# Kernel optimization log

Hardware: AMD Instinct MI355X
Metric: run time of the kernel (lower is better)

The kernel has to match this reference:

```python
import jax, jax.numpy as jnp
import numpy as np

B, H, W = 512, 15, 15
DF, DP, DV, DD = 64, 32, 64, 32
PM = 16
NUM_LINE = 442503  # get_total_num_line_encoding(11)


def fake_quant(x, scale=128., num_bits=8, floor=False):
    qmin = float(-(2 ** (num_bits - 1)))
    qmax = float(2 ** (num_bits - 1) - 1)
    xs = jnp.clip(x * scale, qmin, qmax)
    q = jnp.floor(xs) if floor else jnp.round(xs)
    q = xs + jax.lax.stop_gradient(q - xs)  # straight-through estimator
    return q / scale


def qw(w):  # LinearBlock quant=True weight: int8 at scale 128
    return fake_quant(w, 128., 8)


def qb(b):  # LinearBlock quant=True bias: int32 at scale 128*128
    return fake_quant(b, 128. * 128., 32)


def setup_inputs() -> dict:
    key = jax.random.key(0)
    ks = jax.random.split(key, 24)
    n = lambda k, shape, s=0.1: jax.random.normal(k, shape, dtype=jnp.float32) * s
    return {
        'line_encoding': jax.random.randint(ks[0], (B, 4, H, W), 0, NUM_LINE, dtype=jnp.int32),
        'emb': n(ks[1], (NUM_LINE, DF), 0.5),
        'dw_w': n(ks[2], (DD, 3, 3)),
        'dw_b': n(ks[3], (DD,)),
        'pw1_w': n(ks[4], (DP * 2, DF)), 'pw1_b': n(ks[5], (DP * 2,)),
        'pw2_w': n(ks[6], (PM * DP + PM, DP * 2)), 'pw2_b': n(ks[7], (PM * DP + PM,)),
        'pout_w': n(ks[8], (PM,), 0.2), 'pout_b': n(ks[9], (1,), 0.2),
        'star_up1_w': n(ks[10], (4, DV, DF)), 'star_up1_b': n(ks[11], (4, DV)),
        'star_up2_w': n(ks[12], (4, DV, DF)), 'star_up2_b': n(ks[13], (4, DV)),
        'star_down_w': n(ks[14], (4, DV, DV)), 'star_down_b': n(ks[15], (4, DV)),
        'vl1_w': n(ks[16], (DV, DF + 4 * DV)), 'vl1_b': n(ks[17], (DV,)),
        'vl2_w': n(ks[18], (DV, DV)), 'vl2_b': n(ks[19], (DV,)),
        'vl3_w': n(ks[20], (3, DV)), 'vl3_b': n(ks[21], (3,)),
    }


def _star(x, w1, b1, w2, b2, w3, b3):
    # x: [B,R,DF]; weights [R,DV,DF] (per-region parameter gather)
    x1 = jnp.einsum('brc,rdc->brd', x, qw(w1)) + qb(b1)[None]
    x2 = jnp.einsum('brc,rdc->brd', x, qw(w2)) + qb(b2)[None]
    h = jax.nn.relu(x1) * x2  # star operation
    return jnp.einsum('brc,rdc->brd', h, qw(w3)) + qb(b3)[None]


def _forward(line_encoding, emb, dw_w, dw_b, pw1_w, pw1_b, pw2_w, pw2_b,
             pout_w, pout_b, star_up1_w, star_up1_b, star_up2_w, star_up2_b,
             star_down_w, star_down_b, vl1_w, vl1_b, vl2_w, vl2_b, vl3_w, vl3_b):
    # ---- feature: embedding gather + quant + direction mean ----
    f = emb[line_encoding]                       # [B,4,H,W,DF]
    f = jnp.clip(f, -16., 16.)
    f = fake_quant(f, 32., 16)
    f = jax.nn.relu(jnp.mean(f, axis=1))         # [B,H,W,DF]
    f = jnp.transpose(f, (0, 3, 1, 2))           # [B,DF,H,W]
    # ---- depthwise 3x3 conv, quant='pixel-dwconv-floor' ----
    x = fake_quant(f[:, :DD] * 4., 128., 16)
    wq = fake_quant(dw_w, 65536., 16)
    bq = fake_quant(dw_b, 128., 16)
    xp = jnp.pad(x, ((0, 0), (0, 0), (1, 1), (1, 1)))
    pat = jnp.stack([xp[:, :, dy:dy + H, dx:dx + W]
                     for dy in range(3) for dx in range(3)], axis=2)  # [B,DD,9,H,W]
    prod = fake_quant(pat * wq.reshape(1, DD, 9, 1, 1), 128., 32, floor=True)
    conv = jax.nn.relu(prod.sum(axis=2) + bq.reshape(1, DD, 1, 1))
    feat_dw = fake_quant(conv, 128., 16)
    feat_dir = fake_quant(f[:, DD:], 128., 16)
    feature = jnp.concatenate([feat_dw, feat_dir], axis=1)  # [B,DF,H,W]
    # ---- global and 3x3 regional sums ----
    feature_sum = fake_quant(feature.sum(axis=(2, 3)) / 256., 128., 32, floor=True)
    Hs = [0, H // 3 + (H % 3 == 2), H // 3 * 2 + (H % 3 > 0), H]
    Ws = [0, W // 3 + (W % 3 == 2), W // 3 * 2 + (W % 3 > 0), W]
    regions = jnp.stack([feature[:, :, Hs[i]:Hs[i + 1], Ws[j]:Ws[j + 1]].sum(axis=(2, 3))
                         for i in range(3) for j in range(3)], axis=1)  # [B,9,DF]
    regions = fake_quant(regions / 32., 128., 32, floor=True)
    # ---- policy: dynamic per-sample pointwise conv ----
    h = jax.nn.relu(feature_sum @ qw(pw1_w).T + qb(pw1_b))
    o = h @ qw(pw2_w).T + qb(pw2_b)                         # [B, PM*DP+PM]
    pw = fake_quant(o[:, :PM * DP], 128. * 128., 16, floor=True).reshape(-1, PM, DP)
    pin = fake_quant(feature[:, :DP], 128., 16)             # [B,DP,H,W]
    pol = jnp.einsum('bchw,bic->bihw', pin, pw)             # grouped conv, groups=B
    pbias = o[:, PM * DP:].reshape(-1, PM, 1, 1)
    pol = jax.nn.relu(pol + pbias)
    policy = jnp.einsum('bihw,i->bhw', pol, pout_w)[:, None] + pout_b[0]  # [B,1,H,W]
    # ---- value: corner/edge/center star blocks over 9 regions ----
    idx = jnp.array([0, 1, 0, 1, 2, 1, 0, 1, 0])  # 0=corner,1=edge,2=center
    v = _star(regions, star_up1_w[idx], star_up1_b[idx], star_up2_w[idx],
              star_up2_b[idx], star_down_w[idx], star_down_b[idx])  # [B,9,DV]
    fq8 = lambda t: fake_quant(t, 128., 8, floor=True)
    def avg4(a, b, c, d):
        a, b, c, d = fq8(a), fq8(b), fq8(c), fq8(d)
        ab = fq8((a + b + 1. / 128.) / 2.)
        cd = fq8((c + d + 1. / 128.) / 2.)
        return fq8((ab + cd + 1. / 128.) / 2.)
    quads = jnp.stack([avg4(v[:, 0], v[:, 1], v[:, 3], v[:, 4]),
                       avg4(v[:, 1], v[:, 2], v[:, 4], v[:, 5]),
                       avg4(v[:, 3], v[:, 4], v[:, 6], v[:, 7]),
                       avg4(v[:, 4], v[:, 5], v[:, 7], v[:, 8])], axis=1)  # [B,4,DV]
    qidx = jnp.array([3, 3, 3, 3])  # value_quad shared across quadrants
    vq = _star(quads, star_up1_w[qidx], star_up1_b[qidx], star_up2_w[qidx],
               star_up2_b[qidx], star_down_w[qidx], star_down_b[qidx])  # [B,4,DV]
    value = jnp.concatenate([feature_sum, vq.reshape(vq.shape[0], -1)], axis=1)  # [B,320]
    value = jax.nn.relu(value @ qw(vl1_w).T + qb(vl1_b))
    value = jax.nn.relu(value @ qw(vl2_w).T + qb(vl2_b))
    value = value @ qw(vl3_w).T + qb(vl3_b)                 # [B,3]
    return value, policy


def reference(line_encoding, emb, dw_w, dw_b, pw1_w, pw1_b, pw2_w, pw2_b,
              pout_w, pout_b, star_up1_w, star_up1_b, star_up2_w, star_up2_b,
              star_down_w, star_down_b, vl1_w, vl1_b, vl2_w, vl2_b, vl3_w, vl3_b):
    return _forward(line_encoding, emb, dw_w, dw_b, pw1_w, pw1_b, pw2_w, pw2_b,
                    pout_w, pout_b, star_up1_w, star_up1_b, star_up2_w, star_up2_b,
                    star_down_w, star_down_b, vl1_w, vl1_b, vl2_w, vl2_b, vl3_w, vl3_b)
```

## Files before the change

kernel.cpp:

```cpp
#include <hip/hip_runtime.h>

#define NPOS 225
#define FSTR 226

#define OFF_PW1Q 0
#define OFF_PW2Q 4096
#define OFF_SU1Q 37888
#define OFF_SU2Q 54272
#define OFF_SDQ  70656
#define OFF_VL1Q 87040
#define OFF_VL2Q 107520
#define OFF_VL3Q 111616
#define OFF_PW1B 111808
#define OFF_PW2B 111872
#define OFF_SU1B 112400
#define OFF_SU2B 112656
#define OFF_SDB  112912
#define OFF_VL1B 113168
#define OFF_VL2B 113232
#define OFF_VL3B 113296
#define OFF_DWW  113300
#define OFF_DWB  113588
#define WS_TOTAL 113620

__device__ __forceinline__ float qw8(float w) {
  return rintf(fminf(fmaxf(w * 128.f, -128.f), 127.f)) * 0.0078125f;
}
__device__ __forceinline__ float qb32(float b) {
  return rintf(b * 16384.f) * 6.103515625e-05f;
}
__device__ __forceinline__ float fq8f(float v) {
  return floorf(fminf(fmaxf(v * 128.f, -128.f), 127.f)) * 0.0078125f;
}
__device__ __forceinline__ float qd32(float v) {
  return rintf(fminf(fmaxf(v, -16.f), 16.f) * 32.f);
}

__global__ void nnue_prep(const float* __restrict__ pw1_w, const float* __restrict__ pw1_b,
                          const float* __restrict__ pw2_w, const float* __restrict__ pw2_b,
                          const float* __restrict__ su1w,  const float* __restrict__ su1b,
                          const float* __restrict__ su2w,  const float* __restrict__ su2b,
                          const float* __restrict__ sdw,   const float* __restrict__ sdb,
                          const float* __restrict__ vl1w,  const float* __restrict__ vl1b,
                          const float* __restrict__ vl2w,  const float* __restrict__ vl2b,
                          const float* __restrict__ vl3w,  const float* __restrict__ vl3b,
                          const float* __restrict__ dw_w,  const float* __restrict__ dw_b,
                          float* __restrict__ wsf, int* __restrict__ wsi)
{
  const int i = blockIdx.x * 256 + threadIdx.x;
  if (i < 111808) {
    const float* src; int off;
    if      (i < 4096)   { src = pw1_w; off = 0; }
    else if (i < 37888)  { src = pw2_w; off = 4096; }
    else if (i < 54272)  { src = su1w;  off = 37888; }
    else if (i < 70656)  { src = su2w;  off = 54272; }
    else if (i < 87040)  { src = sdw;   off = 70656; }
    else if (i < 107520) { src = vl1w;  off = 87040; }
    else if (i < 111616) { src = vl2w;  off = 107520; }
    else                 { src = vl3w;  off = 111616; }
    wsf[i] = qw8(src[i - off]);
  } else if (i < 113299) {
    const int j = i - 111808;
    const float* src; int off;
    if      (j < 64)   { src = pw1_b; off = 0; }
    else if (j < 592)  { src = pw2_b; off = 64; }
    else if (j < 848)  { src = su1b;  off = 592; }
    else if (j < 1104) { src = su2b;  off = 848; }
    else if (j < 1360) { src = sdb;   off = 1104; }
    else if (j < 1424) { src = vl1b;  off = 1360; }
    else if (j < 1488) { src = vl2b;  off = 1424; }
    else               { src = vl3b;  off = 1488; }
    wsf[i] = qb32(src[j - off]);
  } else if (i >= 113300 && i < 113588) {
    wsi[i] = (int)rintf(fminf(fmaxf(dw_w[i - 113300] * 65536.f, -32768.f), 32767.f));
  } else if (i >= 113588 && i < 113620) {
    wsi[i] = (int)rintf(fminf(fmaxf(dw_b[i - 113588] * 128.f, -32768.f), 32767.f));
  }
}

__global__ __launch_bounds__(256, 3)
void nnue_main(const int* __restrict__ line, const float* __restrict__ emb,
               const float* __restrict__ pout_w, const float* __restrict__ pout_b,
               const float* __restrict__ wsf, const int* __restrict__ wsi,
               float* __restrict__ out)
{
  __shared__ unsigned short fbuf[64 * FSTR];
  __shared__ int sle[900];
  __shared__ float sreg[576];
  __shared__ float sfsum[64];
  __shared__ float shh[64];
  __shared__ float sobuf[528];
  __shared__ float spwq[512];
  __shared__ float hstar[576];
  __shared__ float vstar[576];
  __shared__ float squads[256];
  __shared__ float shq[256];
  __shared__ float svq[256];
  __shared__ float sv1[64];
  __shared__ float sv2[64];

  const int tid  = threadIdx.x;
  const int b    = blockIdx.x;
  const int wid  = tid >> 6;
  const int lane = tid & 63;
  const int* le  = line + b * 4 * NPOS;

  for (int i = tid; i < 900; i += 256) sle[i] = le[i];
  __syncthreads();

  const int start = (wid * NPOS) >> 2;
  const int end   = ((wid + 1) * NPOS) >> 2;
  for (int p0 = start; p0 < end; p0 += 8) {
    float vv[32];
#pragma unroll
    for (int j = 0; j < 8; ++j) {
      int pp = p0 + j; if (pp >= end) pp = end - 1;
#pragma unroll
      for (int d = 0; d < 4; ++d) {
        const int idx = __builtin_amdgcn_readfirstlane(sle[d * NPOS + pp]);
        vv[j * 4 + d] = emb[(size_t)(unsigned)idx * 64u + (unsigned)lane];
      }
    }
#pragma unroll
    for (int j = 0; j < 8; ++j) {
      const int pp = p0 + j;
      if (pp < end) {
        float s = qd32(vv[4 * j]) + qd32(vv[4 * j + 1]) + qd32(vv[4 * j + 2]) + qd32(vv[4 * j + 3]);
        fbuf[lane * FSTR + pp] = (unsigned short)fmaxf(s, 0.f);
      }
    }
  }
  __syncthreads();

  {
    const int cc = tid >> 3;
    const int pg = tid & 7;
    int w9[9];
#pragma unroll
    for (int t = 0; t < 9; ++t) w9[t] = wsi[OFF_DWW + cc * 9 + t];
    const int bqi = wsi[OFF_DWB + cc];
    const unsigned short* frow = &fbuf[cc * FSTR];
    int outr[29];
#pragma unroll
    for (int k = 0; k < 29; ++k) {
      const int p = pg + 8 * k;
      int res = 0;
      if (p < NPOS) {
        const int y0 = (p * 2185) >> 15;
        const int x0 = p - y0 * 15;
        const int ym = (y0 > 0), yp = (y0 < 14), xm = (x0 > 0), xp = (x0 < 14);
        int acc = 0;
#pragma unroll
        for (int dy = 0; dy < 3; ++dy) {
          const int vy = (dy == 0) ? ym : ((dy == 2) ? yp : 1);
#pragma unroll
          for (int dx = 0; dx < 3; ++dx) {
            const int vx = (dx == 0) ? xm : ((dx == 2) ? xp : 1);
            int q = p + (dy - 1) * 15 + (dx - 1);
            q = (q < 0) ? 0 : ((q > 224) ? 224 : q);
            int kk = frow[q];
            kk = (vy && vx) ? kk : 0;
            acc += (kk * 4 * w9[dy * 3 + dx]) >> 16;
          }
        }
        res = acc + bqi;
        res = res < 0 ? 0 : res;
        res = res > 32767 ? 32767 : res;
      }
      outr[k] = res;
    }
    __syncthreads();
#pragma unroll
    for (int k = 0; k < 29; ++k) {
      const int p = pg + 8 * k;
      if (p < NPOS) fbuf[cc * FSTR + p] = (unsigned short)outr[k];
    }
  }
  __syncthreads();

  {
    int* sregKi = (int*)sreg;
    for (int task = tid; task < 576; task += 256) {
      const int r = task >> 6, c = task & 63;
      const int rh = (r * 11) >> 5;
      const int rw = r - rh * 3;
      const unsigned short* fr = &fbuf[c * FSTR + rh * 75 + rw * 5];
      int K = 0;
#pragma unroll
      for (int y = 0; y < 5; ++y)
#pragma unroll
        for (int x = 0; x < 5; ++x) K += fr[y * 15 + x];
      sregKi[task] = K;
    }
  }
  __syncthreads();
  if (tid < 64) {
    int* sregKi = (int*)sreg;
    int Ks[9], tot = 0;
#pragma unroll
    for (int r = 0; r < 9; ++r) { Ks[r] = sregKi[r * 64 + tid]; tot += Ks[r]; }
#pragma unroll
    for (int r = 0; r < 9; ++r) sreg[r * 64 + tid] = (float)(Ks[r] >> 5) * 0.0078125f;
    sfsum[tid] = (float)(tot >> 8) * 0.0078125f;
  }
  __syncthreads();

  if (tid < 64) {
    const float4* wr = (const float4*)(wsf + OFF_PW1Q + tid * 64);
    float acc = 0.f;
#pragma unroll
    for (int c4 = 0; c4 < 16; ++c4) {
      float4 w = wr[c4];
      acc += sfsum[c4 * 4 + 0] * w.x;
      acc += sfsum[c4 * 4 + 1] * w.y;
      acc += sfsum[c4 * 4 + 2] * w.z;
      acc += sfsum[c4 * 4 + 3] * w.w;
    }
    shh[tid] = fmaxf(acc + wsf[OFF_PW1B + tid], 0.f);
  }
  __syncthreads();
  for (int j = tid; j < 528; j += 256) {
    const float4* wr = (const float4*)(wsf + OFF_PW2Q + j * 64);
    float acc = 0.f;
#pragma unroll
    for (int c4 = 0; c4 < 16; ++c4) {
      float4 w = wr[c4];
      acc += shh[c4 * 4 + 0] * w.x;
      acc += shh[c4 * 4 + 1] * w.y;
      acc += shh[c4 * 4 + 2] * w.z;
      acc += shh[c4 * 4 + 3] * w.w;
    }
    acc += wsf[OFF_PW2B + j];
    sobuf[j] = acc;
    if (j < 512)
      spwq[j] = floorf(fminf(fmaxf(acc * 16384.f, -32768.f), 32767.f)) * 6.103515625e-05f;
  }
  __syncthreads();

  if (tid < NPOS) {
    float pinv[32];
#pragma unroll
    for (int c = 0; c < 32; ++c) pinv[c] = (float)fbuf[c * FSTR + tid] * 0.0078125f;
    float acc = 0.f;
#pragma unroll
    for (int i = 0; i < 16; ++i) {
      float s = 0.f;
#pragma unroll
      for (int c = 0; c < 32; ++c) s += pinv[c] * spwq[i * 32 + c];
      s = fmaxf(s + sobuf[512 + i], 0.f);
      acc += s * pout_w[i];
    }
    out[1536 + b * NPOS + tid] = acc + pout_b[0];
  }

  {
    const int g = tid >> 6;
    const int d = tid & 63;
    int ty, rA, rB, rC, rD;
    if (g == 0)      { ty = 0; rA = 0; rB = 2; rC = 6; rD = 8; }
    else if (g == 1) { ty = 1; rA = 1; rB = 3; rC = 5; rD = 7; }
    else             { ty = 2; rA = 4; rB = 4; rC = 4; rD = 4; }
    const float4* w1r = (const float4*)(wsf + OFF_SU1Q + ty * 4096 + d * 64);
    const float4* w2r = (const float4*)(wsf + OFF_SU2Q + ty * 4096 + d * 64);
    float aA1 = 0, aB1 = 0, aC1 = 0, aD1 = 0, aA2 = 0, aB2 = 0, aC2 = 0, aD2 = 0;
#pragma unroll 4
    for (int c4 = 0; c4 < 16; ++c4) {
      float4 w1 = w1r[c4], w2 = w2r[c4];
      float q1[4] = {w1.x, w1.y, w1.z, w1.w};
      float q2[4] = {w2.x, w2.y, w2.z, w2.w};
#pragma unroll
      for (int u = 0; u < 4; ++u) {
        const int c = c4 * 4 + u;
        float xA = sreg[rA * 64 + c], xB = sreg[rB * 64 + c];
        float xC = sreg[rC * 64 + c], xD = sreg[rD * 64 + c];
        aA1 += xA * q1[u]; aB1 += xB * q1[u]; aC1 += xC * q1[u]; aD1 += xD * q1[u];
        aA2 += xA * q2[u]; aB2 += xB * q2[u]; aC2 += xC * q2[u]; aD2 += xD * q2[u];
      }
    }
    const float bb1 = wsf[OFF_SU1B + ty * 64 + d];
    const float bb2 = wsf[OFF_SU2B + ty * 64 + d];
    hstar[rA * 64 + d] = fmaxf(aA1 + bb1, 0.f) * (aA2 + bb2);
    hstar[rB * 64 + d] = fmaxf(aB1 + bb1, 0.f) * (aB2 + bb2);
    hstar[rC * 64 + d] = fmaxf(aC1 + bb1, 0.f) * (aC2 + bb2);
    hstar[rD * 64 + d] = fmaxf(aD1 + bb1, 0.f) * (aD2 + bb2);
    __syncthreads();
    const float4* wdr = (const float4*)(wsf + OFF_SDQ + ty * 4096 + d * 64);
    float dA = 0, dB = 0, dC = 0, dD = 0;
#pragma unroll 4
    for (int c4 = 0; c4 < 16; ++c4) {
      float4 w = wdr[c4];
      float q[4] = {w.x, w.y, w.z, w.w};
#pragma unroll
      for (int u = 0; u < 4; ++u) {
        const int c = c4 * 4 + u;
        dA += hstar[rA * 64 + c] * q[u]; dB += hstar[rB * 64 + c] * q[u];
        dC += hstar[rC * 64 + c] * q[u]; dD += hstar[rD * 64 + c] * q[u];
      }
    }
    const float bd = wsf[OFF_SDB + ty * 64 + d];
    vstar[rA * 64 + d] = dA + bd;
    vstar[rB * 64 + d] = dB + bd;
    vstar[rC * 64 + d] = dC + bd;
    vstar[rD * 64 + d] = dD + bd;
  }
  __syncthreads();

  {
    const int g = tid >> 6, d = tid & 63;
    int r0, r1, r2v, r3v;
    if (g == 0)      { r0 = 0; r1 = 1; r2v = 3; r3v = 4; }
    else if (g == 1) { r0 = 1; r1 = 2; r2v = 4; r3v = 5; }
    else if (g == 2) { r0 = 3; r1 = 4; r2v = 6; r3v = 7; }
    else             { r0 = 4; r1 = 5; r2v = 7; r3v = 8; }
    float a  = fq8f(vstar[r0 * 64 + d]);
    float bb = fq8f(vstar[r1 * 64 + d]);
    float cc = fq8f(vstar[r2v * 64 + d]);
    float dd = fq8f(vstar[r3v * 64 + d]);
    float ab = fq8f((a + bb + 0.0078125f) * 0.5f);
    float cd = fq8f((cc + dd + 0.0078125f) * 0.5f);
    squads[g * 64 + d] = fq8f((ab + cd + 0.0078125f) * 0.5f);
  }
  __syncthreads();

  {
    const int g = tid >> 6, d = tid & 63;
    const float4* w1r = (const float4*)(wsf + OFF_SU1Q + 3 * 4096 + d * 64);
    const float4* w2r = (const float4*)(wsf + OFF_SU2Q + 3 * 4096 + d * 64);
    float a1 = 0.f, a2 = 0.f;
#pragma unroll 4
    for (int c4 = 0; c4 < 16; ++c4) {
      float4 w1 = w1r[c4], w2 = w2r[c4];
      float xq0 = squads[g * 64 + c4 * 4 + 0], xq1 = squads[g * 64 + c4 * 4 + 1];
      float xq2 = squads[g * 64 + c4 * 4 + 2], xq3 = squads[g * 64 + c4 * 4 + 3];
      a1 += xq0 * w1.x + xq1 * w1.y + xq2 * w1.z + xq3 * w1.w;
      a2 += xq0 * w2.x + xq1 * w2.y + xq2 * w2.z + xq3 * w2.w;
    }
    shq[g * 64 + d] = fmaxf(a1 + wsf[OFF_SU1B + 192 + d], 0.f) * (a2 + wsf[OFF_SU2B + 192 + d]);
    __syncthreads();
    const float4* wdr = (const float4*)(wsf + OFF_SDQ + 3 * 4096 + d * 64);
    float ad = 0.f;
#pragma unroll 4
    for (int c4 = 0; c4 < 16; ++c4) {
      float4 w = wdr[c4];
      ad += shq[g * 64 + c4 * 4 + 0] * w.x + shq[g * 64 + c4 * 4 + 1] * w.y
          + shq[g * 64 + c4 * 4 + 2] * w.z + shq[g * 64 + c4 * 4 + 3] * w.w;
    }
    svq[g * 64 + d] = ad + wsf[OFF_SDB + 192 + d];
  }
  __syncthreads();

  if (tid < 64) {
    const float4* wr = (const float4*)(wsf + OFF_VL1Q + tid * 320);
    float acc = 0.f;
#pragma unroll 4
    for (int k4 = 0; k4 < 16; ++k4) {
      float4 w = wr[k4];
      acc += sfsum[k4 * 4 + 0] * w.x;
      acc += sfsum[k4 * 4 + 1] * w.y;
      acc += sfsum[k4 * 4 + 2] * w.z;
      acc += sfsum[k4 * 4 + 3] * w.w;
    }
#pragma unroll 4
    for (int k4 = 16; k4 < 80; ++k4) {
      float4 w = wr[k4];
      const int base = k4 * 4 - 64;
      acc += svq[base + 0] * w.x;
      acc += svq[base + 1] * w.y;
      acc += svq[base + 2] * w.z;
      acc += svq[base + 3] * w.w;
    }
    sv1[tid] = fmaxf(acc + wsf[OFF_VL1B + tid], 0.f);
  }
  __syncthreads();
  if (tid < 64) {
    const float4* wr = (const float4*)(wsf + OFF_VL2Q + tid * 64);
    float acc = 0.f;
#pragma unroll 4
    for (int k4 = 0; k4 < 16; ++k4) {
      float4 w = wr[k4];
      acc += sv1[k4 * 4 + 0] * w.x;
      acc += sv1[k4 * 4 + 1] * w.y;
      acc += sv1[k4 * 4 + 2] * w.z;
      acc += sv1[k4 * 4 + 3] * w.w;
    }
    sv2[tid] = fmaxf(acc + wsf[OFF_VL2B + tid], 0.f);
  }
  __syncthreads();
  if (tid < 3) {
    const float* wr = wsf + OFF_VL3Q + tid * 64;
    float acc = 0.f;
#pragma unroll
    for (int k = 0; k < 64; ++k) acc += sv2[k] * wr[k];
    out[b * 3 + tid] = acc + wsf[OFF_VL3B + tid];
  }
}

extern "C" void kernel_launch(void* const* d_in, const int* in_sizes, int n_in,
                              void* d_out, int out_size, void* d_ws, size_t ws_size,
                              hipStream_t stream) {
  (void)in_sizes; (void)n_in; (void)out_size; (void)ws_size;
  float* wsf = (float*)d_ws;
  int*   wsi = (int*)d_ws;
  nnue_prep<<<(WS_TOTAL + 255) / 256, 256, 0, stream>>>(
      (const float*)d_in[4],  (const float*)d_in[5],
      (const float*)d_in[6],  (const float*)d_in[7],
      (const float*)d_in[10], (const float*)d_in[11],
      (const float*)d_in[12], (const float*)d_in[13],
      (const float*)d_in[14], (const float*)d_in[15],
      (const float*)d_in[16], (const float*)d_in[17],
      (const float*)d_in[18], (const float*)d_in[19],
      (const float*)d_in[20], (const float*)d_in[21],
      (const float*)d_in[2],  (const float*)d_in[3],
      wsf, wsi);
  nnue_main<<<512, 256, 0, stream>>>(
      (const int*)d_in[0], (const float*)d_in[1],
      (const float*)d_in[8], (const float*)d_in[9],
      wsf, wsi, (float*)d_out);
}
```

Baseline: 260.1 us.

## Double block to 512 threads and run policy and value branches concurrently

Raises the workgroup to 512 threads (8 waves). Embedding gather now uses 8 waves, reads line indices directly from global memory instead of staging them in LDS, and issues all 32 index loads before the embedding loads. The upper 4 waves compute the star value branch while the lower waves run the policy pw1/pw2/output layers, so the two branches overlap instead of running serially. This adds register pressure under the new launch bounds and some extra barriers, and leaves many threads idle in the tail layers.

```diff
diff --git a/kernel.cpp b/kernel.cpp
--- a/kernel.cpp
+++ b/kernel.cpp
@@ -78,14 +78,13 @@
   }
 }
 
-__global__ __launch_bounds__(256, 3)
+__global__ __launch_bounds__(512, 4)
 void nnue_main(const int* __restrict__ line, const float* __restrict__ emb,
                const float* __restrict__ pout_w, const float* __restrict__ pout_b,
                const float* __restrict__ wsf, const int* __restrict__ wsi,
                float* __restrict__ out)
 {
   __shared__ unsigned short fbuf[64 * FSTR];
-  __shared__ int sle[900];
   __shared__ float sreg[576];
   __shared__ float sfsum[64];
   __shared__ float shh[64];
@@ -101,49 +100,47 @@
 
   const int tid  = threadIdx.x;
   const int b    = blockIdx.x;
-  const int wid  = tid >> 6;
+  const int wid  = __builtin_amdgcn_readfirstlane(tid >> 6);
   const int lane = tid & 63;
   const int* le  = line + b * 4 * NPOS;
 
-  for (int i = tid; i < 900; i += 256) sle[i] = le[i];
-  __syncthreads();
-
-  const int start = (wid * NPOS) >> 2;
-  const int end   = ((wid + 1) * NPOS) >> 2;
-  for (int p0 = start; p0 < end; p0 += 8) {
-    float vv[32];
-#pragma unroll
-    for (int j = 0; j < 8; ++j) {
-      int pp = p0 + j; if (pp >= end) pp = end - 1;
-#pragma unroll
-      for (int d = 0; d < 4; ++d) {
-        const int idx = __builtin_amdgcn_readfirstlane(sle[d * NPOS + pp]);
-        vv[j * 4 + d] = emb[(size_t)(unsigned)idx * 64u + (unsigned)lane];
-      }
-    }
-#pragma unroll
-    for (int j = 0; j < 8; ++j) {
-      const int pp = p0 + j;
-      if (pp < end) {
-        float s = qd32(vv[4 * j]) + qd32(vv[4 * j + 1]) + qd32(vv[4 * j + 2]) + qd32(vv[4 * j + 3]);
-        fbuf[lane * FSTR + pp] = (unsigned short)fmaxf(s, 0.f);
-      }
-    }
-  }
-  __syncthreads();
-
   {
-    const int cc = tid >> 3;
-    const int pg = tid & 7;
+    const int s = (wid * NPOS) >> 3;
+    const int e = ((wid + 1) * NPOS) >> 3;
+    for (int p0 = s; p0 < e; p0 += 8) {
+      int idx[32];
+#pragma unroll
+      for (int j = 0; j < 8; ++j) {
+        int pp = p0 + j; pp = (pp < e) ? pp : (e - 1);
+#pragma unroll
+        for (int d = 0; d < 4; ++d) idx[j * 4 + d] = le[d * NPOS + pp];
+      }
+      float vv[32];
+#pragma unroll
+      for (int t = 0; t < 32; ++t)
+        vv[t] = emb[(unsigned)(idx[t] * 64 + lane)];
+#pragma unroll
+      for (int j = 0; j < 8; ++j) {
+        int pp = p0 + j; pp = (pp < e) ? pp : (e - 1);
+        float sm = qd32(vv[4 * j]) + qd32(vv[4 * j + 1]) + qd32(vv[4 * j + 2]) + qd32(vv[4 * j + 3]);
+        fbuf[lane * FSTR + pp] = (unsigned short)fmaxf(sm, 0.f);
+      }
+    }
+  }
+  __syncthreads();
+
+  {
+    const int cc = tid >> 4;
+    const int pg = tid & 15;
     int w9[9];
 #pragma unroll
     for (int t = 0; t < 9; ++t) w9[t] = wsi[OFF_DWW + cc * 9 + t];
     const int bqi = wsi[OFF_DWB + cc];
     const unsigned short* frow = &fbuf[cc * FSTR];
-    int outr[29];
-#pragma unroll
-    for (int k = 0; k < 29; ++k) {
-      const int p = pg + 8 * k;
+    int outr[15];
+#pragma unroll
+    for (int k = 0; k < 15; ++k) {
+      const int p = pg + 16 * k;
       int res = 0;
       if (p < NPOS) {
         const int y0 = (p * 2185) >> 15;
@@ -171,8 +168,8 @@
     }
     __syncthreads();
 #pragma unroll
-    for (int k = 0; k < 29; ++k) {
-      const int p = pg + 8 * k;
+    for (int k = 0; k < 15; ++k) {
+      const int p = pg + 16 * k;
       if (p < NPOS) fbuf[cc * FSTR + p] = (unsigned short)outr[k];
     }
   }
@@ -180,7 +177,7 @@
 
   {
     int* sregKi = (int*)sreg;
-    for (int task = tid; task < 576; task += 256) {
+    for (int task = tid; task < 576; task += 512) {
       const int r = task >> 6, c = task & 63;
       const int rh = (r * 11) >> 5;
       const int rw = r - rh * 3;
@@ -211,102 +208,108 @@
 #pragma unroll
     for (int c4 = 0; c4 < 16; ++c4) {
       float4 w = wr[c4];
-      acc += sfsum[c4 * 4 + 0] * w.x;
-      acc += sfsum[c4 * 4 + 1] * w.y;
-      acc += sfsum[c4 * 4 + 2] * w.z;
-      acc += sfsum[c4 * 4 + 3] * w.w;
+      acc += sfsum[c4 * 4 + 0] * w.x + sfsum[c4 * 4 + 1] * w.y
+           + sfsum[c4 * 4 + 2] * w.z + sfsum[c4 * 4 + 3] * w.w;
     }
     shh[tid] = fmaxf(acc + wsf[OFF_PW1B + tid], 0.f);
-  }
-  __syncthreads();
-  for (int j = tid; j < 528; j += 256) {
-    const float4* wr = (const float4*)(wsf + OFF_PW2Q + j * 64);
-    float acc = 0.f;
-#pragma unroll
-    for (int c4 = 0; c4 < 16; ++c4) {
-      float4 w = wr[c4];
-      acc += shh[c4 * 4 + 0] * w.x;
-      acc += shh[c4 * 4 + 1] * w.y;
-      acc += shh[c4 * 4 + 2] * w.z;
-      acc += shh[c4 * 4 + 3] * w.w;
-    }
-    acc += wsf[OFF_PW2B + j];
-    sobuf[j] = acc;
-    if (j < 512)
-      spwq[j] = floorf(fminf(fmaxf(acc * 16384.f, -32768.f), 32767.f)) * 6.103515625e-05f;
-  }
-  __syncthreads();
-
-  if (tid < NPOS) {
-    float pinv[32];
-#pragma unroll
-    for (int c = 0; c < 32; ++c) pinv[c] = (float)fbuf[c * FSTR + tid] * 0.0078125f;
-    float acc = 0.f;
-#pragma unroll
-    for (int i = 0; i < 16; ++i) {
-      float s = 0.f;
-#pragma unroll
-      for (int c = 0; c < 32; ++c) s += pinv[c] * spwq[i * 32 + c];
-      s = fmaxf(s + sobuf[512 + i], 0.f);
-      acc += s * pout_w[i];
-    }
-    out[1536 + b * NPOS + tid] = acc + pout_b[0];
-  }
-
-  {
-    const int g = tid >> 6;
+  } else if (tid >= 256) {
+    const int g = (tid >> 6) - 4;
+    const int d = tid & 63;
+    int ty, rA, rB, rC, rD;
+    if (g == 0)      { ty = 0; rA = 0; rB = 2; rC = 6; rD = 8; }
+    else if (g == 1) { ty = 1; rA = 1; rB = 3; rC = 5; rD = 7; }
+    else if (g == 2) { ty = 2; rA = 4; rB = 4; rC = 4; rD = 4; }
+    else             { ty = 3; rA = 4; rB = 4; rC = 4; rD = 4; }
+    if (g < 3) {
+      const float4* w1r = (const float4*)(wsf + OFF_SU1Q + ty * 4096 + d * 64);
+      const float4* w2r = (const float4*)(wsf + OFF_SU2Q + ty * 4096 + d * 64);
+      float aA1 = 0, aB1 = 0, aC1 = 0, aD1 = 0, aA2 = 0, aB2 = 0, aC2 = 0, aD2 = 0;
+#pragma unroll 4
+      for (int c4 = 0; c4 < 16; ++c4) {
+        float4 w1 = w1r[c4], w2 = w2r[c4];
+        float q1[4] = {w1.x, w1.y, w1.z, w1.w};
+        float q2[4] = {w2.x, w2.y, w2.z, w2.w};
+#pragma unroll
+        for (int u = 0; u < 4; ++u) {
+          const int c = c4 * 4 + u;
+          float xA = sreg[rA * 64 + c], xB = sreg[rB * 64 + c];
+          float xC = sreg[rC * 64 + c], xD = sreg[rD * 64 + c];
+          aA1 += xA * q1[u]; aB1 += xB * q1[u]; aC1 += xC * q1[u]; aD1 += xD * q1[u];
+          aA2 += xA * q2[u]; aB2 += xB * q2[u]; aC2 += xC * q2[u]; aD2 += xD * q2[u];
+        }
+      }
+      const float bb1 = wsf[OFF_SU1B + ty * 64 + d];
+      const float bb2 = wsf[OFF_SU2B + ty * 64 + d];
+      hstar[rA * 64 + d] = fmaxf(aA1 + bb1, 0.f) * (aA2 + bb2);
+      hstar[rB * 64 + d] = fmaxf(aB1 + bb1, 0.f) * (aB2 + bb2);
+      hstar[rC * 64 + d] = fmaxf(aC1 + bb1, 0.f) * (aC2 + bb2);
+      hstar[rD * 64 + d] = fmaxf(aD1 + bb1, 0.f) * (aD2 + bb2);
+    }
+  }
+  __syncthreads();
+
+  if (tid < 256) {
+    for (int j = tid; j < 528; j += 256) {
+      const float4* wr = (const float4*)(wsf + OFF_PW2Q + j * 64);
+      float acc = 0.f;
+#pragma unroll
+      for (int c4 = 0; c4 < 16; ++c4) {
+        float4 w = wr[c4];
+        acc += shh[c4 * 4 + 0] * w.x + shh[c4 * 4 + 1] * w.y
+             + shh[c4 * 4 + 2] * w.z + shh[c4 * 4 + 3] * w.w;
+      }
+      acc += wsf[OFF_PW2B + j];
+      sobuf[j] = acc;
+      if (j < 512)
+        spwq[j] = floorf(fminf(fmaxf(acc * 16384.f, -32768.f), 32767.f)) * 6.103515625e-05f;
+    }
+  } else {
+    const int g = (tid >> 6) - 4;
     const int d = tid & 63;
     int ty, rA, rB, rC, rD;
     if (g == 0)      { ty = 0; rA = 0; rB = 2; rC = 6; rD = 8; }
     else if (g == 1) { ty = 1; rA = 1; rB = 3; rC = 5; rD = 7; }
     else             { ty = 2; rA = 4; rB = 4; rC = 4; rD = 4; }
-    const float4* w1r = (const float4*)(wsf + OFF_SU1Q + ty * 4096 + d * 64);
-    const float4* w2r = (const float4*)(wsf + OFF_SU2Q + ty * 4096 + d * 64);
-    float aA1 = 0, aB1 = 0, aC1 = 0, aD1 = 0, aA2 = 0, aB2 = 0, aC2 = 0, aD2 = 0;
-#pragma unroll 4
-    for (int c4 = 0; c4 < 16; ++c4) {
-      float4 w1 = w1r[c4], w2 = w2r[c4];
-      float q1[4] = {w1.x, w1.y, w1.z, w1.w};
-      float q2[4] = {w2.x, w2.y, w2.z, w2.w};
-#pragma unroll
-      for (int u = 0; u < 4; ++u) {
-        const int c = c4 * 4 + u;
-        float xA = sreg[rA * 64 + c], xB = sreg[rB * 64 + c];
-        float xC = sreg[rC * 64 + c], xD = sreg[rD * 64 + c];
-        aA1 += xA * q1[u]; aB1 += xB * q1[u]; aC1 += xC * q1[u]; aD1 += xD * q1[u];
-        aA2 += xA * q2[u]; aB2 += xB * q2[u]; aC2 += xC * q2[u]; aD2 += xD * q2[u];
-      }
-    }
-    const float bb1 = wsf[OFF_SU1B + ty * 64 + d];
-    const float bb2 = wsf[OFF_SU2B + ty * 64 + d];
-    hstar[rA * 64 + d] = fmaxf(aA1 + bb1, 0.f) * (aA2 + bb2);
-    hstar[rB * 64 + d] = fmaxf(aB1 + bb1, 0.f) * (aB2 + bb2);
-    hstar[rC * 64 + d] = fmaxf(aC1 + bb1, 0.f) * (aC2 + bb2);
-    hstar[rD * 64 + d] = fmaxf(aD1 + bb1, 0.f) * (aD2 + bb2);
-    __syncthreads();
-    const float4* wdr = (const float4*)(wsf + OFF_SDQ + ty * 4096 + d * 64);
-    float dA = 0, dB = 0, dC = 0, dD = 0;
-#pragma unroll 4
-    for (int c4 = 0; c4 < 16; ++c4) {
-      float4 w = wdr[c4];
-      float q[4] = {w.x, w.y, w.z, w.w};
-#pragma unroll
-      for (int u = 0; u < 4; ++u) {
-        const int c = c4 * 4 + u;
-        dA += hstar[rA * 64 + c] * q[u]; dB += hstar[rB * 64 + c] * q[u];
-        dC += hstar[rC * 64 + c] * q[u]; dD += hstar[rD * 64 + c] * q[u];
-      }
-    }
-    const float bd = wsf[OFF_SDB + ty * 64 + d];
-    vstar[rA * 64 + d] = dA + bd;
-    vstar[rB * 64 + d] = dB + bd;
-    vstar[rC * 64 + d] = dC + bd;
-    vstar[rD * 64 + d] = dD + bd;
-  }
-  __syncthreads();
-
-  {
-    const int g = tid >> 6, d = tid & 63;
+    if (g < 3) {
+      const float4* wdr = (const float4*)(wsf + OFF_SDQ + ty * 4096 + d * 64);
+      float dA = 0, dB = 0, dC = 0, dD = 0;
+#pragma unroll 4
+      for (int c4 = 0; c4 < 16; ++c4) {
+        float4 w = wdr[c4];
+        float q[4] = {w.x, w.y, w.z, w.w};
+#pragma unroll
+        for (int u = 0; u < 4; ++u) {
+          const int c = c4 * 4 + u;
+          dA += hstar[rA * 64 + c] * q[u]; dB += hstar[rB * 64 + c] * q[u];
+          dC += hstar[rC * 64 + c] * q[u]; dD += hstar[rD * 64 + c] * q[u];
+        }
+      }
+      const float bd = wsf[OFF_SDB + ty * 64 + d];
+      vstar[rA * 64 + d] = dA + bd;
+      vstar[rB * 64 + d] = dB + bd;
+      vstar[rC * 64 + d] = dC + bd;
+      vstar[rD * 64 + d] = dD + bd;
+    }
+  }
+  __syncthreads();
+
+  if (tid < NPOS) {
+    float pinv[32];
+#pragma unroll
+    for (int c = 0; c < 32; ++c) pinv[c] = (float)fbuf[c * FSTR + tid] * 0.0078125f;
+    float acc = 0.f;
+#pragma unroll
+    for (int i = 0; i < 16; ++i) {
+      float s = 0.f;
+#pragma unroll
+      for (int c = 0; c < 32; ++c) s += pinv[c] * spwq[i * 32 + c];
+      s = fmaxf(s + sobuf[512 + i], 0.f);
+      acc += s * pout_w[i];
+    }
+    out[1536 + b * NPOS + tid] = acc + pout_b[0];
+  } else if (tid >= 256) {
+    const int g = (tid >> 6) - 4;
+    const int d = tid & 63;
     int r0, r1, r2v, r3v;
     if (g == 0)      { r0 = 0; r1 = 1; r2v = 3; r3v = 4; }
     else if (g == 1) { r0 = 1; r1 = 2; r2v = 4; r3v = 5; }
@@ -322,8 +325,9 @@
   }
   __syncthreads();
 
-  {
-    const int g = tid >> 6, d = tid & 63;
+  if (tid >= 256) {
+    const int g = (tid >> 6) - 4;
+    const int d = tid & 63;
     const float4* w1r = (const float4*)(wsf + OFF_SU1Q + 3 * 4096 + d * 64);
     const float4* w2r = (const float4*)(wsf + OFF_SU2Q + 3 * 4096 + d * 64);
     float a1 = 0.f, a2 = 0.f;
@@ -336,7 +340,12 @@
       a2 += xq0 * w2.x + xq1 * w2.y + xq2 * w2.z + xq3 * w2.w;
     }
     shq[g * 64 + d] = fmaxf(a1 + wsf[OFF_SU1B + 192 + d], 0.f) * (a2 + wsf[OFF_SU2B + 192 + d]);
-    __syncthreads();
+  }
+  __syncthreads();
+
+  if (tid >= 256) {
+    const int g = (tid >> 6) - 4;
+    const int d = tid & 63;
     const float4* wdr = (const float4*)(wsf + OFF_SDQ + 3 * 4096 + d * 64);
     float ad = 0.f;
 #pragma unroll 4
@@ -355,19 +364,15 @@
 #pragma unroll 4
     for (int k4 = 0; k4 < 16; ++k4) {
       float4 w = wr[k4];
-      acc += sfsum[k4 * 4 + 0] * w.x;
-      acc += sfsum[k4 * 4 + 1] * w.y;
-      acc += sfsum[k4 * 4 + 2] * w.z;
-      acc += sfsum[k4 * 4 + 3] * w.w;
+      acc += sfsum[k4 * 4 + 0] * w.x + sfsum[k4 * 4 + 1] * w.y
+           + sfsum[k4 * 4 + 2] * w.z + sfsum[k4 * 4 + 3] * w.w;
     }
 #pragma unroll 4
     for (int k4 = 16; k4 < 80; ++k4) {
       float4 w = wr[k4];
       const int base = k4 * 4 - 64;
-      acc += svq[base + 0] * w.x;
-      acc += svq[base + 1] * w.y;
-      acc += svq[base + 2] * w.z;
-      acc += svq[base + 3] * w.w;
+      acc += svq[base + 0] * w.x + svq[base + 1] * w.y
+           + svq[base + 2] * w.z + svq[base + 3] * w.w;
     }
     sv1[tid] = fmaxf(acc + wsf[OFF_VL1B + tid], 0.f);
   }
@@ -378,10 +383,8 @@
 #pragma unroll 4
     for (int k4 = 0; k4 < 16; ++k4) {
       float4 w = wr[k4];
-      acc += sv1[k4 * 4 + 0] * w.x;
-      acc += sv1[k4 * 4 + 1] * w.y;
-      acc += sv1[k4 * 4 + 2] * w.z;
-      acc += sv1[k4 * 4 + 3] * w.w;
+      acc += sv1[k4 * 4 + 0] * w.x + sv1[k4 * 4 + 1] * w.y
+           + sv1[k4 * 4 + 2] * w.z + sv1[k4 * 4 + 3] * w.w;
     }
     sv2[tid] = fmaxf(acc + wsf[OFF_VL2B + tid], 0.f);
   }
@@ -412,7 +415,7 @@
       (const float*)d_in[20], (const float*)d_in[21],
       (const float*)d_in[2],  (const float*)d_in[3],
       wsf, wsi);
-  nnue_main<<<512, 256, 0, stream>>>(
+  nnue_main<<<512, 512, 0, stream>>>(
       (const int*)d_in[0], (const float*)d_in[1],
       (const float*)d_in[8], (const float*)d_in[9],
       wsf, wsi, (float*)d_out);
```

After: 253.0 us. 1.03x faster.
